# Optimization experiments

Hardware: AMD Instinct MI355X
Metric: run time of the kernel (lower is better)

Reference implementation:

```python
import jax, jax.numpy as jnp
import numpy as np

B, M, N, R, FD = 128, 64, 64, 8, 128
BN_EPS = 1e-5
GS_EPS = 1e-8


def conv2d(x, w, b):
    # x: [B,C,H,W], w: [O,C,3,3] or [O,C,1,1]
    y = jax.lax.conv_general_dilated(x, w, (1, 1), 'SAME',
                                     dimension_numbers=('NCHW', 'OIHW', 'NCHW'))
    return y + b[None, :, None, None]


def complex_conv(x, wr, br, wi, bi):
    cr = conv2d(x, wr, br)
    ci = conv2d(x, wi, bi)
    return jnp.concatenate([cr - ci, cr + ci], axis=1)


def batchnorm(x, g, b):
    # training-mode BN over (B,H,W)
    mean = x.mean(axis=(0, 2, 3), keepdims=True)
    var = ((x - mean) ** 2).mean(axis=(0, 2, 3), keepdims=True)
    return g[None, :, None, None] * (x - mean) * jax.lax.rsqrt(var + BN_EPS) + b[None, :, None, None]


def gram_schmidt(mat):
    # mat: [B, M, R, 2]; sequential over R (hard data dependency), vectorized over batch
    Rr = mat.shape[2]
    basis = []  # list of (vr, vi), each [B, M]
    for j in range(Rr):
        vr, vi = mat[:, :, j, 0], mat[:, :, j, 1]
        for br_, bi_ in basis:
            dot_real = jnp.sum(vr * br_ + vi * bi_, axis=1, keepdims=True)
            denom = jnp.sum(br_ * br_ + bi_ * bi_, axis=1, keepdims=True) + GS_EPS
            coef = dot_real / denom  # only real part used (as in torch code)
            vr = vr - coef * br_
            vi = vi - coef * bi_
        nrm = jnp.sqrt(jnp.sum(vr * vr + vi * vi, axis=1, keepdims=True) + GS_EPS)
        basis.append((vr / nrm, vi / nrm))
    return jnp.stack([jnp.stack(p, axis=-1) for p in basis], axis=2)  # [B,M,R,2]


def setup_inputs() -> dict:
    key = jax.random.key(0)
    ks = jax.random.split(key, 32)
    def p(i, shape, fan_in):
        return jax.random.normal(ks[i], shape, jnp.float32) / np.sqrt(fan_in)
    inp = {
        'x':   jax.random.normal(ks[0], (B, M, N, 2), jnp.float32),
        'w1r': p(1, (32, 2, 3, 3), 2 * 9),   'b1r': jnp.zeros((32,), jnp.float32),
        'w1i': p(2, (32, 2, 3, 3), 2 * 9),   'b1i': jnp.zeros((32,), jnp.float32),
        'g1':  jnp.ones((64,), jnp.float32), 'be1': jnp.zeros((64,), jnp.float32),
        'w2r': p(3, (64, 64, 3, 3), 64 * 9), 'b2r': jnp.zeros((64,), jnp.float32),
        'w2i': p(4, (64, 64, 3, 3), 64 * 9), 'b2i': jnp.zeros((64,), jnp.float32),
        'g2':  jnp.ones((128,), jnp.float32), 'be2': jnp.zeros((128,), jnp.float32),
        'w3r': p(5, (FD, 128, 3, 3), 128 * 9), 'b3r': jnp.zeros((FD,), jnp.float32),
        'w3i': p(6, (FD, 128, 3, 3), 128 * 9), 'b3i': jnp.zeros((FD,), jnp.float32),
        'g3':  jnp.ones((2 * FD,), jnp.float32), 'be3': jnp.zeros((2 * FD,), jnp.float32),
        'wu':  p(7, (2 * R, 2 * FD), 2 * FD), 'bu': jnp.zeros((2 * R,), jnp.float32),
        'ws':  p(8, (R, 2 * FD), 2 * FD),     'bs': jnp.zeros((R,), jnp.float32),
        'wv':  p(9, (2 * R, 2 * FD), 2 * FD), 'bv': jnp.zeros((2 * R,), jnp.float32),
    }
    return inp


def forward(x, w1r, b1r, w1i, b1i, g1, be1, w2r, b2r, w2i, b2i, g2, be2,
            w3r, b3r, w3i, b3i, g3, be3, wu, bu, ws, bs, wv, bv):
    h = jnp.transpose(x, (0, 3, 1, 2))  # [B,2,M,N]
    h = jax.nn.relu(batchnorm(complex_conv(h, w1r, b1r, w1i, b1i), g1, be1))
    h = jax.nn.relu(batchnorm(complex_conv(h, w2r, b2r, w2i, b2i), g2, be2))
    h = jax.nn.relu(batchnorm(complex_conv(h, w3r, b3r, w3i, b3i), g3, be3))  # [B,2FD,M,N]
    # u branch: avg over W, 1x1 conv (= channel matmul), relu
    pu = h.mean(axis=3)                                      # [B,2FD,M]
    u = jax.nn.relu(jnp.einsum('bcm,oc->bom', pu, wu) + bu[None, :, None])  # [B,2R,M]
    u = jnp.transpose(u, (0, 2, 1)).reshape(-1, M, R, 2)     # channel c = 2j+part
    u = gram_schmidt(u)
    # s branch: global avg pool + linear + relu
    ps = h.mean(axis=(2, 3))                                 # [B,2FD]
    s = jax.nn.relu(ps @ ws.T + bs)                          # [B,R]
    # v branch: avg over H, 1x1 conv, relu
    pv = h.mean(axis=2)                                      # [B,2FD,N]
    v = jax.nn.relu(jnp.einsum('bcn,oc->bon', pv, wv) + bv[None, :, None])  # [B,2R,N]
    v = jnp.transpose(v, (0, 2, 1)).reshape(-1, N, R, 2)
    v = gram_schmidt(v)
    return (u, s, v)


def reference(x, w1r, b1r, w1i, b1i, g1, be1, w2r, b2r, w2i, b2i, g2, be2,
              w3r, b3r, w3i, b3i, g3, be3, wu, bu, ws, bs, wv, bv):
    return forward(x, w1r, b1r, w1i, b1i, g1, be1, w2r, b2r, w2i, b2i, g2, be2,
                   w3r, b3r, w3i, b3i, g3, be3, wu, bu, ws, bs, wv, bv)
```

## Files before the change

kernel.cpp:

```cpp
#include <hip/hip_runtime.h>

typedef _Float16 f16;
typedef __attribute__((ext_vector_type(8))) short short8;
typedef __attribute__((ext_vector_type(8))) _Float16 half8;
typedef __attribute__((ext_vector_type(4))) float f32x4;

#define DEV __device__ __forceinline__

DEV float h2f(short s) { f16 h; __builtin_memcpy(&h, &s, 2); return (float)h; }
DEV short f2h(float f) { f16 h = (f16)f; short s; __builtin_memcpy(&s, &h, 2); return s; }
DEV half8 s2h8(short8 s) { half8 h; __builtin_memcpy(&h, &s, 16); return h; }

DEV float wave_sum(float v) {
    #pragma unroll
    for (int m = 1; m < 64; m <<= 1) v += __shfl_xor(v, m);
    return v;
}

__global__ __launch_bounds__(256) void prep_w_k(
    const float* __restrict__ wr, const float* __restrict__ wi,
    f16* __restrict__ wf, int CIN, int COUT)
{
    int idx = blockIdx.x * 256 + threadIdx.x;
    int KC = CIN >> 5, NG = (2 * COUT) >> 4;
    int total = 9 * KC * NG * 512;
    if (idx >= total) return;
    int j = idx & 7, lane = (idx >> 3) & 63;
    int t9 = idx >> 9;
    int gg = t9 % NG, s = t9 / NG;
    int tap = s % 9, kc = s / 9;
    int n = gg * 16 + (lane & 15);
    int cin = kc * 32 + (lane >> 4) * 8 + j;
    int o = n < COUT ? n : n - COUT;
    float sgn = n < COUT ? -1.f : 1.f;
    float wv = wr[(o * CIN + cin) * 9 + tap] + sgn * wi[(o * CIN + cin) * 9 + tap];
    wf[idx] = (f16)wv;
}

__global__ __launch_bounds__(256) void conv1_k(
    const float* __restrict__ x,
    const float* __restrict__ w1r, const float* __restrict__ w1i,
    f16* __restrict__ out)
{
    int idx = blockIdx.x * 256 + threadIdx.x;
    int b = idx >> 12, p = idx & 4095;
    int m = p >> 6, n = p & 63;

    float v[2][9];
    #pragma unroll
    for (int dy = 0; dy < 3; ++dy)
        #pragma unroll
        for (int dx = 0; dx < 3; ++dx) {
            int yy = m + dy - 1, xx = n + dx - 1;
            bool ok = (yy >= 0 && yy < 64 && xx >= 0 && xx < 64);
            int base = ((b * 64 + (ok ? yy : 0)) * 64 + (ok ? xx : 0)) * 2;
            v[0][dy*3+dx] = ok ? x[base]     : 0.f;
            v[1][dy*3+dx] = ok ? x[base + 1] : 0.f;
        }

    float o1[64];
    #pragma unroll
    for (int o = 0; o < 32; ++o) {
        float cr = 0.f, ci = 0.f;
        #pragma unroll
        for (int c = 0; c < 2; ++c)
            #pragma unroll
            for (int k = 0; k < 9; ++k) {
                cr = fmaf(v[c][k], w1r[(o*2+c)*9 + k], cr);
                ci = fmaf(v[c][k], w1i[(o*2+c)*9 + k], ci);
            }
        o1[o]      = cr - ci;
        o1[32 + o] = cr + ci;
    }
    f16* ob = out + (size_t)idx * 64;
    #pragma unroll
    for (int grp = 0; grp < 8; ++grp) {
        short8 pk;
        #pragma unroll
        for (int k = 0; k < 8; ++k) pk[k] = f2h(o1[grp*8 + k]);
        *(short8*)(ob + grp * 8) = pk;
    }
}

template<int C8>
__global__ __launch_bounds__(256) void statsv_k(
    const f16* __restrict__ t, float* __restrict__ stats, int iters)
{
    const int C = C8 * 8;
    __shared__ float ls[2 * C];
    const int tid = threadIdx.x;
    const int cg = tid & (C8 - 1), pg = tid / C8;
    const int NG = 256 / C8;
    for (int u = tid; u < 2 * C; u += 256) ls[u] = 0.f;
    __syncthreads();
    float s8[8] = {0,0,0,0,0,0,0,0}, q8[8] = {0,0,0,0,0,0,0,0};
    size_t base = (size_t)blockIdx.x * NG * iters + pg;
    for (int i = 0; i < iters; ++i) {
        size_t pp = base + (size_t)i * NG;
        short8 r = *(const short8*)(t + pp * C + cg * 8);
        #pragma unroll
        for (int k = 0; k < 8; ++k) { float v = h2f(r[k]); s8[k] += v; q8[k] += v * v; }
    }
    #pragma unroll
    for (int k = 0; k < 8; ++k) {
        atomicAdd(&ls[cg*8 + k], s8[k]);
        atomicAdd(&ls[C + cg*8 + k], q8[k]);
    }
    __syncthreads();
    for (int u = tid; u < C; u += 256) {
        atomicAdd(&stats[u], ls[u]);
        atomicAdd(&stats[C + u], ls[C + u]);
    }
}

__global__ void bnparam_k(const float* __restrict__ stats,
                          const float* __restrict__ g, const float* __restrict__ be,
                          float* __restrict__ sc, int C)
{
    int c = threadIdx.x;
    if (c >= C) return;
    const float invN = 1.f / (128.f * 4096.f);
    float mean  = stats[c] * invN;
    float var   = stats[C + c] * invN - mean * mean;
    float scale = g[c] * rsqrtf(var + 1e-5f);
    sc[c]     = scale;
    sc[C + c] = be[c] - mean * scale;
}

template<int CIN, bool CHUNK>
__global__ __launch_bounds__(512, 2) void conv_mfma_k(
    const f16* __restrict__ in, const f16* __restrict__ wf,
    const float* __restrict__ scin, f16* __restrict__ outp,
    float* __restrict__ stats, int n0, int NG, int statsC, int ostride)
{
    constexpr int KQ = CIN / 32;
    constexpr int NSTEP = KQ * 9;
    constexpr int NH   = CHUNK ? 1 : 2;
    constexpr int RW   = 8 / NH;
    constexpr int ROWS = 2 * RW;
    constexpr int SROWS = ROWS + 2;
    constexpr int YT   = 64 / ROWS;
    __shared__ char actl[SROWS*66*32*2];
    __shared__ float lsts[8][64], lstq[8][64];
    const int flat = blockIdx.x;
    const int swzb = (flat & 7) * (128*YT/8) + (flat >> 3);
    const int b = swzb / YT, y0 = (swzb % YT) * ROWS;
    const int tid = threadIdx.x, l = tid & 63, w = tid >> 6;
    const int rp = w / NH, nh = w % NH;
    const int li = l & 15, g = l >> 4;

    f32x4 acc[8][4];
    #pragma unroll
    for (int mf = 0; mf < 8; ++mf)
        #pragma unroll
        for (int nf = 0; nf < 4; ++nf)
            acc[mf][nf] = f32x4{0.f, 0.f, 0.f, 0.f};

    int swz[3];
    #pragma unroll
    for (int dx = 0; dx < 3; ++dx) swz[dx] = ((li + dx) & 7) << 4;

    const f16* wblk = wf + ((size_t)((n0 >> 4) + nh*4) << 9) + (l << 3);
    auto bload = [&](int st, short8* dst) {
        const f16* p = wblk + ((size_t)(st * NG) << 9);
        #pragma unroll
        for (int nf = 0; nf < 4; ++nf) dst[nf] = *(const short8*)(p + (nf << 9));
    };
    short8 breg[4], nbreg[4];
    bload(0, breg);

    for (int st = 0; st < NSTEP; ++st) {
        const int kq = st / 9, tap = st - kq * 9;
        if (tap == 0) {
            half8 scl8, shf8;
            {
                int cb = kq*32 + (tid & 3) * 8;
                #pragma unroll
                for (int k = 0; k < 8; ++k) {
                    scl8[k] = (f16)scin[cb + k];
                    shf8[k] = (f16)scin[CIN + cb + k];
                }
            }
            __syncthreads();
            #pragma unroll
            for (int i = 0; i < (SROWS*66*4 + 511)/512; ++i) {
                int u = tid + i * 512;
                if (u < SROWS*66*4) {
                    int r = u / 264, rem = u - r * 264;
                    int sx = rem >> 2, cg = rem & 3;
                    int srow = y0 - 1 + r, gx = sx - 1;
                    short8 pk = {0,0,0,0,0,0,0,0};
                    if (srow >= 0 && srow < 64 && gx >= 0 && gx < 64) {
                        short8 raw = *(const short8*)(in +
                            ((size_t)(b*4096 + srow*64 + gx)) * CIN + kq*32 + cg*8);
                        half8 rv = s2h8(raw) * scl8 + shf8;
                        short8 sr; __builtin_memcpy(&sr, &rv, 16);
                        pk = sr & ~(sr >> 15);
                    }
                    int off = ((r*66 + sx)*32 + cg*8)*2 ^ ((sx & 7) << 4);
                    *(short8*)(actl + off) = pk;
                }
            }
            __syncthreads();
        }
        if (st + 1 < NSTEP) bload(st + 1, nbreg);
        int dy = (tap * 11) >> 5, dx = tap - dy * 3;
        __builtin_amdgcn_s_setprio(1);
        #pragma unroll
        for (int mf = 0; mf < 8; ++mf) {
            int r = 2*rp + (mf >> 2) + dy;
            int sx = (mf & 3)*16 + li + dx;
            half8 a = s2h8(*(const short8*)(actl + ((((r*66 + sx)*32) + g*8)*2 ^ swz[dx])));
            #pragma unroll
            for (int nf = 0; nf < 4; ++nf)
                acc[mf][nf] = __builtin_amdgcn_mfma_f32_16x16x32_f16(a, s2h8(breg[nf]), acc[mf][nf], 0, 0, 0);
        }
        __builtin_amdgcn_s_setprio(0);
        #pragma unroll
        for (int nf = 0; nf < 4; ++nf) breg[nf] = nbreg[nf];
    }

    #pragma unroll
    for (int nf = 0; nf < 4; ++nf) {
        float s = 0.f, q = 0.f;
        #pragma unroll
        for (int mf = 0; mf < 8; ++mf)
            #pragma unroll
            for (int reg = 0; reg < 4; ++reg) {
                float v = acc[mf][nf][reg];
                s += v; q += v * v;
            }
        s += __shfl_xor(s, 16); s += __shfl_xor(s, 32);
        q += __shfl_xor(q, 16); q += __shfl_xor(q, 32);
        if (l < 16) { lsts[w][nf*16 + l] = s; lstq[w][nf*16 + l] = q; }
    }
    __syncthreads();
    if (tid < NH*64) {
        int ch64 = tid & 63, half = tid >> 6;
        float s = 0.f, q = 0.f;
        #pragma unroll
        for (int j = 0; j < RW; ++j) {
            s += lsts[j*NH + half][ch64];
            q += lstq[j*NH + half][ch64];
        }
        atomicAdd(&stats[tid], s);
        atomicAdd(&stats[statsC + tid], q);
    }

    const int obase = nh * 64;
    #pragma unroll
    for (int mf = 0; mf < 8; ++mf) {
        size_t rowbase = (size_t)b * 4096 + (size_t)(y0 + 2*rp + (mf >> 2)) * 64;
        #pragma unroll
        for (int nf = 0; nf < 4; ++nf) {
            int n = obase + nf*16 + li;
            #pragma unroll
            for (int reg = 0; reg < 4; ++reg) {
                int xx = (mf & 3)*16 + g*4 + reg;
                outp[(rowbase + xx) * ostride + n] = (f16)acc[mf][nf][reg];
            }
        }
    }
}

__global__ __launch_bounds__(256) void pool_k(
    const f16* __restrict__ t3c, const float* __restrict__ sc3c,
    float* __restrict__ pu, float* __restrict__ pv, int ncb)
{
    const int b = blockIdx.x, yh = blockIdx.y;
    const int t = threadIdx.x, cg = t & 7, xp = t >> 3;
    const int w = t >> 6, lane = t & 63;
    __shared__ float rq[4][16][64];
    float scl[8], shf[8];
    #pragma unroll
    for (int k = 0; k < 8; ++k) { scl[k] = sc3c[cg*8 + k]; shf[k] = sc3c[64 + cg*8 + k]; }
    float colacc[2][8];
    #pragma unroll
    for (int xi = 0; xi < 2; ++xi)
        #pragma unroll
        for (int k = 0; k < 8; ++k) colacc[xi][k] = 0.f;

    for (int yb = 0; yb < 2; ++yb) {
        for (int yy = 0; yy < 16; ++yy) {
            int y = yh*32 + yb*16 + yy;
            float rc[8];
            #pragma unroll
            for (int xi = 0; xi < 2; ++xi) {
                int xx = xp*2 + xi;
                short8 raw = *(const short8*)(t3c +
                    ((size_t)(b*4096 + y*64 + xx)) * 64 + cg*8);
                #pragma unroll
                for (int k = 0; k < 8; ++k) {
                    float v = fmaxf(fmaf(h2f(raw[k]), scl[k], shf[k]), 0.f);
                    colacc[xi][k] += v;
                    rc[k] = xi ? (rc[k] + v) : v;
                }
            }
            #pragma unroll
            for (int k = 0; k < 8; ++k) {
                rc[k] += __shfl_xor(rc[k], 8);
                rc[k] += __shfl_xor(rc[k], 16);
                rc[k] += __shfl_xor(rc[k], 32);
            }
            if (lane < 8) {
                #pragma unroll
                for (int k = 0; k < 8; ++k) rq[w][yy][lane*8 + k] = rc[k];
            }
        }
        __syncthreads();
        for (int u = t; u < 1024; u += 256) {
            int yy = u >> 6, c = u & 63;
            float v = rq[0][yy][c] + rq[1][yy][c] + rq[2][yy][c] + rq[3][yy][c];
            pu[((size_t)b*256 + ncb + c)*64 + (yh*32 + yb*16 + yy)] = v * (1.f/64.f);
        }
        __syncthreads();
    }
    #pragma unroll
    for (int xi = 0; xi < 2; ++xi)
        #pragma unroll
        for (int k = 0; k < 8; ++k)
            atomicAdd(&pv[((size_t)b*256 + ncb + cg*8 + k)*64 + xp*2 + xi],
                      colacc[xi][k] * (1.f/64.f));
}

__global__ __launch_bounds__(256) void headuv_k(
    const float* __restrict__ pool, const float* __restrict__ w,
    const float* __restrict__ bias, float* __restrict__ out)
{
    int b = blockIdx.x;
    int m = threadIdx.x & 63;
    int ob4 = threadIdx.x >> 6;
    float acc[4] = { bias[ob4], bias[ob4+4], bias[ob4+8], bias[ob4+12] };
    const float* pb = pool + (size_t)b * 256 * 64 + m;
    for (int c = 0; c < 256; ++c) {
        float v = pb[c * 64];
        #pragma unroll
        for (int i = 0; i < 4; ++i)
            acc[i] = fmaf(v, w[(ob4 + i*4) * 256 + c], acc[i]);
    }
    float* op = out + (size_t)b * 16 * 64 + m;
    #pragma unroll
    for (int i = 0; i < 4; ++i)
        op[(ob4 + i*4) * 64] = fmaxf(acc[i], 0.f);
}

__global__ __launch_bounds__(64) void heads_s_k(
    const float* __restrict__ pu, const float* __restrict__ wS,
    const float* __restrict__ bS, float* __restrict__ out)
{
    int b = blockIdx.x, lane = threadIdx.x;
    __shared__ float ls[256];
    for (int i = 0; i < 4; ++i) {
        const float* p = pu + ((size_t)b*256 + lane*4 + i) * 64;
        float s = 0.f;
        for (int m = 0; m < 64; ++m) s += p[m];
        ls[lane*4 + i] = s * (1.f/64.f);
    }
    __syncthreads();
    float acc[8] = {0,0,0,0,0,0,0,0};
    for (int c = lane; c < 256; c += 64) {
        float v = ls[c];
        #pragma unroll
        for (int o = 0; o < 8; ++o) acc[o] = fmaf(v, wS[o*256 + c], acc[o]);
    }
    #pragma unroll
    for (int o = 0; o < 8; ++o) acc[o] = wave_sum(acc[o]);
    if (lane == 0) {
        #pragma unroll
        for (int o = 0; o < 8; ++o)
            out[b*8 + o] = fmaxf(acc[o] + bS[o], 0.f);
    }
}

__global__ __launch_bounds__(64) void gs_k(
    const float* __restrict__ pre, float* __restrict__ out)
{
    int b = blockIdx.x, lane = threadIdx.x;
    const float* pb = pre + (size_t)b * 16 * 64 + lane;
    float vr[8], vi[8], den[8];
    #pragma unroll
    for (int j = 0; j < 8; ++j) { vr[j] = pb[(2*j)*64]; vi[j] = pb[(2*j+1)*64]; }

    #pragma unroll
    for (int j = 0; j < 8; ++j) {
        #pragma unroll
        for (int k = 0; k < j; ++k) {
            float d = wave_sum(vr[j]*vr[k] + vi[j]*vi[k]);
            float coef = d / den[k];
            vr[j] = fmaf(-coef, vr[k], vr[j]);
            vi[j] = fmaf(-coef, vi[k], vi[j]);
        }
        float n2 = wave_sum(vr[j]*vr[j] + vi[j]*vi[j]);
        float inv = 1.f / sqrtf(n2 + 1e-8f);
        vr[j] *= inv; vi[j] *= inv;
        float nn = wave_sum(vr[j]*vr[j] + vi[j]*vi[j]);
        den[j] = nn + 1e-8f;
    }
    float* ob = out + (size_t)b * 64 * 16 + lane * 16;
    #pragma unroll
    for (int j = 0; j < 8; ++j) { ob[j*2] = vr[j]; ob[j*2+1] = vi[j]; }
}

extern "C" void kernel_launch(void* const* d_in, const int* in_sizes, int n_in,
                              void* d_out, int out_size, void* d_ws, size_t ws_size,
                              hipStream_t stream)
{
    const float* x   = (const float*)d_in[0];
    const float* w1r = (const float*)d_in[1];
    const float* w1i = (const float*)d_in[3];
    const float* g1  = (const float*)d_in[5];
    const float* be1 = (const float*)d_in[6];
    const float* w2r = (const float*)d_in[7];
    const float* w2i = (const float*)d_in[9];
    const float* g2  = (const float*)d_in[11];
    const float* be2 = (const float*)d_in[12];
    const float* w3r = (const float*)d_in[13];
    const float* w3i = (const float*)d_in[15];
    const float* g3  = (const float*)d_in[17];
    const float* be3 = (const float*)d_in[18];
    const float* wu  = (const float*)d_in[19];
    const float* bu  = (const float*)d_in[20];
    const float* wS  = (const float*)d_in[21];
    const float* bS  = (const float*)d_in[22];
    const float* wv  = (const float*)d_in[23];
    const float* bv  = (const float*)d_in[24];
    float* out = (float*)d_out;

    char* ws = (char*)d_ws;
    f16*   t2     = (f16*)  (ws + 0);
    f16*   t1     = (f16*)  (ws + 134217728);
    f16*   t3c    = (f16*)  (ws + 134217728);
    float* upre   = (float*)(ws + 134217728);
    float* vpre   = (float*)(ws + 134742016);
    float* pu     = (float*)(ws + 201326592);
    float* pv     = (float*)(ws + 209715200);
    f16*   wfrag2 = (f16*)  (ws + 218103808);
    f16*   wfrag3 = (f16*)  (ws + 218103808);
    float* stats  = (float*)(ws + 219283456);
    float* scsh   = (float*)(ws + 219287040);
    float* stats1 = stats,  *stats2 = stats + 128;
    float* sc1    = scsh,   *sc2    = scsh  + 128, *sc3c = scsh + 384;

    hipMemsetAsync(stats, 0, 3584, stream);
    hipMemsetAsync(pv, 0, (size_t)128*256*64*4, stream);

    prep_w_k<<<288, 256, 0, stream>>>(w2r, w2i, wfrag2, 64, 64);

    conv1_k<<<2048, 256, 0, stream>>>(x, w1r, w1i, t1);
    statsv_k<8><<<1024, 256, 0, stream>>>(t1, stats1, 16);
    bnparam_k<<<1, 64, 0, stream>>>(stats1, g1, be1, sc1, 64);

    conv_mfma_k<64, false><<<1024, 512, 0, stream>>>(
        t1, wfrag2, sc1, t2, stats2,
        0, 8, 128, 128);
    bnparam_k<<<1, 128, 0, stream>>>(stats2, g2, be2, sc2, 128);

    prep_w_k<<<1152, 256, 0, stream>>>(w3r, w3i, wfrag3, 128, 128);
    for (int nc = 0; nc < 4; ++nc) {
        conv_mfma_k<128, true><<<512, 512, 0, stream>>>(
            t2, wfrag3, sc2, t3c, stats + 384 + nc*128,
            nc*64, 16, 64, 64);
        bnparam_k<<<1, 64, 0, stream>>>(stats + 384 + nc*128, g3 + nc*64, be3 + nc*64, sc3c, 64);
        pool_k<<<dim3(128, 2), 256, 0, stream>>>(t3c, sc3c, pu, pv, nc*64);
    }

    headuv_k<<<128, 256, 0, stream>>>(pu, wu, bu, upre);
    headuv_k<<<128, 256, 0, stream>>>(pv, wv, bv, vpre);
    heads_s_k<<<128, 64, 0, stream>>>(pu, wS, bS, out + 131072);

    gs_k<<<128, 64, 0, stream>>>(upre, out);
    gs_k<<<128, 64, 0, stream>>>(vpre, out + 132096);
}
```

Baseline: 771.3 us.

## Double-buffer activation tiles in LDS and prefetch next channel chunk during MFMA

Moves the conv kernel from a single LDS activation buffer to a double buffer. Global loads for the next 32-channel chunk are split into two halves issued in registers and interleaved with the nine MFMA tap steps, so load latency can hide behind compute and one of the two barriers per chunk goes away. The A fragments are also loaded into registers before the MFMA burst. This doubles LDS use and raises register pressure, which could cut occupancy under the 512x2 launch bounds.

```diff
diff --git a/kernel.cpp b/kernel.cpp
--- a/kernel.cpp
+++ b/kernel.cpp
@@ -127,6 +127,54 @@
     sc[C + c] = be[c] - mean * scale;
 }
 
+template<int CIN, int E, int CNT, int I0>
+DEV void stage_load(const f16* __restrict__ in, int b, int y0, int kq, int tid,
+                    short8* raw)
+{
+    #pragma unroll
+    for (int i = 0; i < CNT; ++i) {
+        int u = tid + (I0 + i) * 512;
+        if (u < E) {
+            int r = u / 264, rem = u - r * 264;
+            int sx = rem >> 2, cg = rem & 3;
+            int srow = y0 - 1 + r, gx = sx - 1;
+            if (srow >= 0 && srow < 64 && gx >= 0 && gx < 64)
+                raw[i] = *(const short8*)(in +
+                    ((size_t)(b*4096 + srow*64 + gx)) * CIN + kq*32 + cg*8);
+        }
+    }
+}
+
+template<int CIN, int E, int CNT, int I0>
+DEV void stage_write(const float* __restrict__ scin, int y0, int kq, int tid,
+                     const short8* raw, char* dst)
+{
+    half8 scl8, shf8;
+    int cb = kq*32 + (tid & 3) * 8;
+    #pragma unroll
+    for (int k = 0; k < 8; ++k) {
+        scl8[k] = (f16)scin[cb + k];
+        shf8[k] = (f16)scin[CIN + cb + k];
+    }
+    #pragma unroll
+    for (int i = 0; i < CNT; ++i) {
+        int u = tid + (I0 + i) * 512;
+        if (u < E) {
+            int r = u / 264, rem = u - r * 264;
+            int sx = rem >> 2, cg = rem & 3;
+            int srow = y0 - 1 + r, gx = sx - 1;
+            short8 pk = {0,0,0,0,0,0,0,0};
+            if (srow >= 0 && srow < 64 && gx >= 0 && gx < 64) {
+                half8 rv = s2h8(raw[i]) * scl8 + shf8;
+                short8 sr; __builtin_memcpy(&sr, &rv, 16);
+                pk = sr & ~(sr >> 15);
+            }
+            int off = ((r*66 + sx)*32 + cg*8)*2 ^ ((sx & 7) << 4);
+            *(short8*)(dst + off) = pk;
+        }
+    }
+}
+
 template<int CIN, bool CHUNK>
 __global__ __launch_bounds__(512, 2) void conv_mfma_k(
     const f16* __restrict__ in, const f16* __restrict__ wf,
@@ -140,7 +188,11 @@
     constexpr int ROWS = 2 * RW;
     constexpr int SROWS = ROWS + 2;
     constexpr int YT   = 64 / ROWS;
-    __shared__ char actl[SROWS*66*32*2];
+    constexpr int E    = SROWS * 66 * 4;
+    constexpr int C    = (E + 511) / 512;
+    constexpr int C0   = (C + 1) / 2, C1 = C - C0;
+    constexpr int AB   = SROWS * 66 * 32 * 2;
+    __shared__ char actl[2][AB];
     __shared__ float lsts[8][64], lstq[8][64];
     const int flat = blockIdx.x;
     const int swzb = (flat & 7) * (128*YT/8) + (flat >> 3);
@@ -167,57 +219,52 @@
         for (int nf = 0; nf < 4; ++nf) dst[nf] = *(const short8*)(p + (nf << 9));
     };
     short8 breg[4], nbreg[4];
-    bload(0, breg);
-
-    for (int st = 0; st < NSTEP; ++st) {
-        const int kq = st / 9, tap = st - kq * 9;
-        if (tap == 0) {
-            half8 scl8, shf8;
-            {
-                int cb = kq*32 + (tid & 3) * 8;
-                #pragma unroll
-                for (int k = 0; k < 8; ++k) {
-                    scl8[k] = (f16)scin[cb + k];
-                    shf8[k] = (f16)scin[CIN + cb + k];
-                }
-            }
-            __syncthreads();
-            #pragma unroll
-            for (int i = 0; i < (SROWS*66*4 + 511)/512; ++i) {
-                int u = tid + i * 512;
-                if (u < SROWS*66*4) {
-                    int r = u / 264, rem = u - r * 264;
-                    int sx = rem >> 2, cg = rem & 3;
-                    int srow = y0 - 1 + r, gx = sx - 1;
-                    short8 pk = {0,0,0,0,0,0,0,0};
-                    if (srow >= 0 && srow < 64 && gx >= 0 && gx < 64) {
-                        short8 raw = *(const short8*)(in +
-                            ((size_t)(b*4096 + srow*64 + gx)) * CIN + kq*32 + cg*8);
-                        half8 rv = s2h8(raw) * scl8 + shf8;
-                        short8 sr; __builtin_memcpy(&sr, &rv, 16);
-                        pk = sr & ~(sr >> 15);
-                    }
-                    int off = ((r*66 + sx)*32 + cg*8)*2 ^ ((sx & 7) << 4);
-                    *(short8*)(actl + off) = pk;
-                }
-            }
-            __syncthreads();
-        }
+
+    auto STEP = [&](int kq, int tap, const char* act) {
+        int st = kq * 9 + tap;
         if (st + 1 < NSTEP) bload(st + 1, nbreg);
         int dy = (tap * 11) >> 5, dx = tap - dy * 3;
-        __builtin_amdgcn_s_setprio(1);
+        half8 a[8];
         #pragma unroll
         for (int mf = 0; mf < 8; ++mf) {
             int r = 2*rp + (mf >> 2) + dy;
             int sx = (mf & 3)*16 + li + dx;
-            half8 a = s2h8(*(const short8*)(actl + ((((r*66 + sx)*32) + g*8)*2 ^ swz[dx])));
+            a[mf] = s2h8(*(const short8*)(act + ((((r*66 + sx)*32) + g*8)*2 ^ swz[dx])));
+        }
+        __builtin_amdgcn_s_setprio(1);
+        #pragma unroll
+        for (int mf = 0; mf < 8; ++mf)
             #pragma unroll
             for (int nf = 0; nf < 4; ++nf)
-                acc[mf][nf] = __builtin_amdgcn_mfma_f32_16x16x32_f16(a, s2h8(breg[nf]), acc[mf][nf], 0, 0, 0);
-        }
+                acc[mf][nf] = __builtin_amdgcn_mfma_f32_16x16x32_f16(a[mf], s2h8(breg[nf]), acc[mf][nf], 0, 0, 0);
         __builtin_amdgcn_s_setprio(0);
         #pragma unroll
         for (int nf = 0; nf < 4; ++nf) breg[nf] = nbreg[nf];
+    };
+
+    short8 rawA[C0], rawB[C1];
+    stage_load <CIN, E, C0, 0 >(in, b, y0, 0, tid, rawA);
+    stage_load <CIN, E, C1, C0>(in, b, y0, 0, tid, rawB);
+    stage_write<CIN, E, C0, 0 >(scin, y0, 0, tid, rawA, actl[0]);
+    stage_write<CIN, E, C1, C0>(scin, y0, 0, tid, rawB, actl[0]);
+    __syncthreads();
+    bload(0, breg);
+
+    for (int kq = 0; kq < KQ; ++kq) {
+        char* cur = actl[kq & 1];
+        char* nxt = actl[(kq + 1) & 1];
+        const bool pf = (kq + 1 < KQ);
+        if (pf) stage_load<CIN, E, C0, 0>(in, b, y0, kq + 1, tid, rawA);
+        #pragma unroll
+        for (int tap = 0; tap < 4; ++tap) STEP(kq, tap, cur);
+        if (pf) {
+            stage_write<CIN, E, C0, 0 >(scin, y0, kq + 1, tid, rawA, nxt);
+            stage_load <CIN, E, C1, C0>(in, b, y0, kq + 1, tid, rawB);
+        }
+        #pragma unroll
+        for (int tap = 4; tap < 9; ++tap) STEP(kq, tap, cur);
+        if (pf) stage_write<CIN, E, C1, C0>(scin, y0, kq + 1, tid, rawB, nxt);
+        __syncthreads();
     }
 
     #pragma unroll
```

Measured after the change: 1.716 ms. +122.5%, slower.
